# Performance work log

Hardware: AMD Instinct MI355X
Metric: run time of the kernel (lower is better)

Reference implementation:

```python
import jax, jax.numpy as jnp
import numpy as np

SEQ = 8          # sequence_size
C = 128          # in_channels / factor (hidden + input channels)
BN_EPS = 1e-5


def setup_inputs() -> dict:
    key = jax.random.key(0)
    k1, k2 = jax.random.split(key)
    x = jax.random.normal(k1, (32, C, 64, 64), dtype=jnp.float32)          # (B*T, C, H, W)
    w_conv = jax.random.normal(k2, (4 * C, 2 * C, 3, 3), dtype=jnp.float32) * 0.05  # OIHW
    b_conv = jnp.zeros((4 * C,), dtype=jnp.float32)
    gamma = jnp.ones((C,), dtype=jnp.float32)
    beta = jnp.zeros((C,), dtype=jnp.float32)
    run_mean = jnp.zeros((C,), dtype=jnp.float32)
    run_var = jnp.ones((C,), dtype=jnp.float32)
    return {"x": x, "w_conv": w_conv, "b_conv": b_conv, "gamma": gamma,
            "beta": beta, "run_mean": run_mean, "run_var": run_var}


def _convlstm_scan(x_seq, w_conv, b_conv):
    # x_seq: (B, T, C, H, W); zero initial (h, c) states (reset path)
    B, T, Cc, H, W = x_seq.shape
    h0 = jnp.zeros((B, Cc, H, W), x_seq.dtype)
    c0 = jnp.zeros((B, Cc, H, W), x_seq.dtype)

    def step(carry, x_t):
        h, c = carry
        z = jax.lax.conv_general_dilated(
            jnp.concatenate([x_t, h], axis=1), w_conv,
            window_strides=(1, 1), padding='SAME',
            dimension_numbers=('NCHW', 'OIHW', 'NCHW'))
        z = z + b_conv[None, :, None, None]
        i, f, o, g = jnp.split(z, 4, axis=1)
        c_next = jax.nn.sigmoid(f) * c + jax.nn.sigmoid(i) * jnp.tanh(g)
        h_next = jax.nn.sigmoid(o) * jnp.tanh(c_next)
        return (h_next, c_next), h_next

    _, hs = jax.lax.scan(step, (h0, c0), jnp.swapaxes(x_seq, 0, 1))  # hs: (T, B, C, H, W)
    return jnp.swapaxes(hs, 0, 1)  # (B, T, C, H, W)


def reference(x, w_conv, b_conv, gamma, beta, run_mean, run_var):
    BT, Cc, H, W = x.shape
    x_seq = x.reshape(BT // SEQ, SEQ, Cc, H, W)
    hs = _convlstm_scan(x_seq, w_conv, b_conv)           # (B, T, C, H, W)
    out = hs.reshape(-1, Cc, H, W)                        # (B*T, C, H, W)
    # BatchNorm2d (eval mode: running stats) + ReLU
    inv = jax.lax.rsqrt(run_var + BN_EPS)
    out = (out - run_mean[None, :, None, None]) * (inv * gamma)[None, :, None, None] \
          + beta[None, :, None, None]
    return jax.nn.relu(out)
```

## Files before the change

### kernel.cpp

```cpp
#include <hip/hip_runtime.h>
#include <hip/hip_bf16.h>
#include <math.h>

typedef __attribute__((ext_vector_type(8))) short bf16x8;
typedef __attribute__((ext_vector_type(4))) float f32x4;

#define FRAME_PAD (66*66*128)

#define GLOAD_LDS16(g, l) \
    __builtin_amdgcn_global_load_lds((const __attribute__((address_space(1))) void*)(g), \
                                     (__attribute__((address_space(3))) void*)(l), 16, 0, 0)

#define WAITV6    asm volatile("s_waitcnt vmcnt(6)" ::: "memory")
#define WAITV0    asm volatile("s_waitcnt vmcnt(0)" ::: "memory")
#define SBAR      __builtin_amdgcn_s_barrier()
#define MEMPIN    asm volatile("" ::: "memory")

__device__ __forceinline__ float sigmoidf_(float x) { return 1.0f / (1.0f + __expf(-x)); }
__device__ __forceinline__ float tanhf_(float x) {
    x = fminf(fmaxf(x, -15.0f), 15.0f);
    float e = __expf(2.0f * x);
    return (e - 1.0f) / (e + 1.0f);
}
__device__ __forceinline__ float b2f_(short u) {
    unsigned int v = ((unsigned int)(unsigned short)u) << 16;
    return __builtin_bit_cast(float, v);
}
__device__ __forceinline__ short f2b_(float f) {
    __hip_bfloat16 hb = __float2bfloat16(f);
    return *reinterpret_cast<short*>(&hb);
}

__global__ void wt_kernel(const float* __restrict__ w, __hip_bfloat16* __restrict__ wt)
{
    int idx = blockIdx.x * 256 + threadIdx.x;
    if (idx >= 9 * 512 * 256) return;
    int ic  = idx & 255;
    int n   = (idx >> 8) & 511;
    int tap = idx >> 17;
    int c = n >> 2, g = n & 3;
    int oc = g * 128 + c;
    wt[idx] = __float2bfloat16(w[((size_t)oc * 256 + (size_t)ic) * 9 + tap]);
}

__global__ void border_kernel(__hip_bfloat16* __restrict__ x_pad,
                              __hip_bfloat16* __restrict__ h_pad)
{
    const int fr = blockIdx.x;
    __hip_bfloat16* base = (fr < 32) ? x_pad + (size_t)fr * FRAME_PAD
                                     : h_pad + (size_t)(fr - 32) * FRAME_PAD;
    bf16x8 z = {};
    for (int u = threadIdx.x; u < 2112; u += 256) {
        int half = (u >= 1056) ? 1 : 0;
        int v = u - half * 1056;
        *(bf16x8*)(base + (size_t)(half * 65 * 66) * 128 + (size_t)v * 8) = z;
    }
    for (int u = threadIdx.x; u < 2048; u += 256) {
        int yy = 1 + (u >> 5);
        int r = u & 31;
        int side = r >> 4, c16 = r & 15;
        *(bf16x8*)(base + (size_t)(yy * 66 + side * 65) * 128 + (size_t)c16 * 8) = z;
    }
}

__global__ void xpose_kernel(const float* __restrict__ x, __hip_bfloat16* __restrict__ x_pad)
{
    __shared__ float tile[64][129];
    const int f = blockIdx.x >> 6;
    const int y = blockIdx.x & 63;
    const int tid = threadIdx.x;
    const float* src = x + (size_t)f * 524288 + (size_t)y * 64;
    #pragma unroll
    for (int it = 0; it < 8; ++it) {
        int c  = it * 16 + (tid >> 4);
        int xq = tid & 15;
        float4 v = *(const float4*)(src + (size_t)c * 4096 + xq * 4);
        tile[xq * 4 + 0][c] = v.x;
        tile[xq * 4 + 1][c] = v.y;
        tile[xq * 4 + 2][c] = v.z;
        tile[xq * 4 + 3][c] = v.w;
    }
    __syncthreads();
    __hip_bfloat16* dst = x_pad + (size_t)f * FRAME_PAD + (size_t)((y + 1) * 66 + 1) * 128;
    const int g = tid & 15;
    #pragma unroll
    for (int it = 0; it < 4; ++it) {
        int xr = it * 16 + (tid >> 4);
        bf16x8 o;
        #pragma unroll
        for (int e = 0; e < 8; ++e) o[e] = f2b_(tile[xr][g * 8 + e]);
        *(bf16x8*)(dst + (size_t)xr * 128 + g * 8) = o;
    }
}

template<bool T0>
__global__ __launch_bounds__(512, 2)
void conv_gemm(const __hip_bfloat16* __restrict__ x_pad,
               const __hip_bfloat16* __restrict__ h_pad,
               const __hip_bfloat16* __restrict__ wt,
               const float* __restrict__ bias,
               float* __restrict__ c_state, int t)
{
    __shared__ alignas(16) __hip_bfloat16 S_s[3][256 * 64];
    __shared__ alignas(16) __hip_bfloat16 W_s[3][128 * 64];
    const int tid  = threadIdx.x;
    const int wv   = tid >> 6;
    const int lane = tid & 63;
    const int KT   = T0 ? 18 : 36;

    const int F    = blockIdx.x;
    const int tile = (F >> 3) + (F & 7) * 32;
    const int n0   = (tile & 3) * 128;
    const int mblk = tile >> 2;
    const int b    = mblk >> 4;
    const int y0   = (mblk & 15) * 4;
    const int m0   = mblk * 256;

    const __hip_bfloat16* xf = x_pad + (size_t)(b * 8 + t) * FRAME_PAD;
    const __hip_bfloat16* hf = h_pad + (size_t)(b * 8 + (T0 ? 0 : t - 1)) * FRAME_PAD;

    int aOff[4], bOff[2];
    #pragma unroll
    for (int j = 0; j < 4; ++j) {
        int sid = j * 512 + tid;
        int row = sid >> 3;
        int q   = (sid & 7) ^ (row & 7);
        aOff[j] = ((y0 + (row >> 6)) * 66 + (row & 63)) * 128 + q * 8;
    }
    #pragma unroll
    for (int j = 0; j < 2; ++j) {
        int sid = j * 512 + tid;
        int row = sid >> 3;
        int q   = (sid & 7) ^ (row & 7);
        bOff[j] = (n0 + row) * 256 + q * 8;
    }

    auto STAGE = [&](__hip_bfloat16* Sl, __hip_bfloat16* Wl, int kt) {
        int tap, icq;
        const __hip_bfloat16* sb;
        if constexpr (T0) { tap = kt >> 1; icq = (kt & 1) * 64; sb = xf + icq; }
        else { tap = kt >> 2; icq = (kt & 3) * 64;
               sb = (icq < 128) ? (xf + icq) : (hf + (icq - 128)); }
        const int dy = tap / 3, dx = tap % 3;
        const __hip_bfloat16* a = sb + (dy * 66 + dx) * 128;
        #pragma unroll
        for (int j = 0; j < 4; ++j)
            GLOAD_LDS16(a + aOff[j], Sl + (size_t)(j * 512 + tid) * 8);
        const __hip_bfloat16* bsrc = wt + tap * 131072 + icq;
        #pragma unroll
        for (int j = 0; j < 2; ++j)
            GLOAD_LDS16(bsrc + bOff[j], Wl + (size_t)(j * 512 + tid) * 8);
    };

    const int wm = wv >> 1, wn = wv & 1;
    const int fr = lane & 15, fq = lane >> 4;
    const int slot = (fq ^ (fr & 7)) * 8;
    const int sOff0 = (wm * 64 + fr) * 64 + slot, sOff1 = sOff0 ^ 32;
    const int wOff0 = (wn * 64 + fr) * 64 + slot, wOff1 = wOff0 ^ 32;

    f32x4 acc[4][4] = {};

    __hip_bfloat16 *Sr = &S_s[0][0], *Sn = &S_s[1][0], *Sf = &S_s[2][0];
    __hip_bfloat16 *Wr = &W_s[0][0], *Wn = &W_s[1][0], *Wf = &W_s[2][0];

    STAGE(Sr, Wr, 0);
    STAGE(Sn, Wn, 1);

    #pragma unroll 1
    for (int kt = 0; kt < KT; ++kt) {
        if (kt < KT - 1) { WAITV6; } else { WAITV0; }
        SBAR;
        MEMPIN;
        if (kt < KT - 2) STAGE(Sf, Wf, kt + 2);

        bf16x8 w0[4], w1[4], s0[4], s1[4];
        #pragma unroll
        for (int ri = 0; ri < 4; ++ri) {
            w0[ri] = *(const bf16x8*)(Wr + wOff0 + ri * 1024);
            w1[ri] = *(const bf16x8*)(Wr + wOff1 + ri * 1024);
        }
        #pragma unroll
        for (int ci = 0; ci < 4; ++ci) {
            s0[ci] = *(const bf16x8*)(Sr + sOff0 + ci * 1024);
            s1[ci] = *(const bf16x8*)(Sr + sOff1 + ci * 1024);
        }
        __builtin_amdgcn_s_setprio(1);
        #pragma unroll
        for (int ri = 0; ri < 4; ++ri)
            #pragma unroll
            for (int ci = 0; ci < 4; ++ci)
                acc[ri][ci] = __builtin_amdgcn_mfma_f32_16x16x32_bf16(w0[ri], s0[ci], acc[ri][ci], 0, 0, 0);
        #pragma unroll
        for (int ri = 0; ri < 4; ++ri)
            #pragma unroll
            for (int ci = 0; ci < 4; ++ci)
                acc[ri][ci] = __builtin_amdgcn_mfma_f32_16x16x32_bf16(w1[ri], s1[ci], acc[ri][ci], 0, 0, 0);
        __builtin_amdgcn_s_setprio(0);

        __hip_bfloat16* tp = Sr; Sr = Sn; Sn = Sf; Sf = tp;
        __hip_bfloat16* tw = Wr; Wr = Wn; Wn = Wf; Wf = tw;
    }

    const int c0    = (n0 >> 2) + wn * 16;
    const int mcol0 = m0 + wm * 64 + fr;
    __hip_bfloat16* hout = (__hip_bfloat16*)h_pad + (size_t)(b * 8 + t) * FRAME_PAD;
    #pragma unroll
    for (int ri = 0; ri < 4; ++ri) {
        const int c = c0 + ri * 4 + fq;
        const float bi  = bias[c];
        const float bfv = bias[128 + c];
        const float bo  = bias[256 + c];
        const float bg  = bias[384 + c];
        float* csrow = c_state + (size_t)c * 16384;
        #pragma unroll
        for (int ci = 0; ci < 4; ++ci) {
            const int m = mcol0 + ci * 16;
            const int s = m & 4095;
            const float cold = T0 ? 0.0f : csrow[m];
            const float zi = acc[ri][ci][0] + bi;
            const float zf = acc[ri][ci][1] + bfv;
            const float zo = acc[ri][ci][2] + bo;
            const float zg = acc[ri][ci][3] + bg;
            const float cn = sigmoidf_(zf) * cold + sigmoidf_(zi) * tanhf_(zg);
            const float h  = sigmoidf_(zo) * tanhf_(cn);
            csrow[m] = cn;
            hout[(size_t)(((s >> 6) + 1) * 66 + (s & 63) + 1) * 128 + c] = __float2bfloat16(h);
        }
    }
}

__global__ void bn_out_kernel(const __hip_bfloat16* __restrict__ h_pad,
                              const float* __restrict__ gamma, const float* __restrict__ beta,
                              const float* __restrict__ rmean, const float* __restrict__ rvar,
                              float* __restrict__ out)
{
    __shared__ float tile[64][129];
    __shared__ float sc_s[128], sh_s[128];
    const int fo  = blockIdx.x >> 6;
    const int y   = blockIdx.x & 63;
    const int tid = threadIdx.x;
    if (tid < 128) {
        float sc = gamma[tid] * rsqrtf(rvar[tid] + 1e-5f);
        sc_s[tid] = sc;
        sh_s[tid] = beta[tid] - rmean[tid] * sc;
    }
    __syncthreads();
    const __hip_bfloat16* src =
        h_pad + (size_t)fo * FRAME_PAD + (size_t)((y + 1) * 66 + 1) * 128;
    const int g = tid & 15;
    float sc[8], sh[8];
    #pragma unroll
    for (int e = 0; e < 8; ++e) { sc[e] = sc_s[g * 8 + e]; sh[e] = sh_s[g * 8 + e]; }
    #pragma unroll
    for (int it = 0; it < 4; ++it) {
        int xr = it * 16 + (tid >> 4);
        bf16x8 v = *(const bf16x8*)(src + (size_t)xr * 128 + g * 8);
        #pragma unroll
        for (int e = 0; e < 8; ++e)
            tile[xr][g * 8 + e] = fmaxf(b2f_(v[e]) * sc[e] + sh[e], 0.0f);
    }
    __syncthreads();
    float* dst = out + (size_t)fo * 524288 + (size_t)y * 64;
    #pragma unroll
    for (int it = 0; it < 8; ++it) {
        int c  = it * 16 + (tid >> 4);
        int xq = tid & 15;
        float4 o;
        o.x = tile[xq * 4 + 0][c];
        o.y = tile[xq * 4 + 1][c];
        o.z = tile[xq * 4 + 2][c];
        o.w = tile[xq * 4 + 3][c];
        *(float4*)(dst + (size_t)c * 4096 + xq * 4) = o;
    }
}

extern "C" void kernel_launch(void* const* d_in, const int* in_sizes, int n_in,
                              void* d_out, int out_size, void* d_ws, size_t ws_size,
                              hipStream_t stream)
{
    const float* x      = (const float*)d_in[0];
    const float* w_conv = (const float*)d_in[1];
    const float* b_conv = (const float*)d_in[2];
    const float* gamma  = (const float*)d_in[3];
    const float* beta   = (const float*)d_in[4];
    const float* rmean  = (const float*)d_in[5];
    const float* rvar   = (const float*)d_in[6];
    float* out = (float*)d_out;

    if (ws_size < 82116608u) return;

    char* ws = (char*)d_ws;
    __hip_bfloat16* Wt    = (__hip_bfloat16*)(ws);
    __hip_bfloat16* x_pad = (__hip_bfloat16*)(ws + 2359296);
    __hip_bfloat16* h_pad = (__hip_bfloat16*)(ws + 38043648);
    float* c_state        = (float*)(ws + 73728000);

    wt_kernel<<<4608, 256, 0, stream>>>(w_conv, Wt);
    xpose_kernel<<<2048, 256, 0, stream>>>(x, x_pad);
    border_kernel<<<64, 256, 0, stream>>>(x_pad, h_pad);

    conv_gemm<true><<<256, 512, 0, stream>>>(x_pad, h_pad, Wt, b_conv, c_state, 0);
    for (int t = 1; t < 8; ++t)
        conv_gemm<false><<<256, 512, 0, stream>>>(x_pad, h_pad, Wt, b_conv, c_state, t);

    bn_out_kernel<<<2048, 256, 0, stream>>>(h_pad, gamma, beta, rmean, rvar, out);
}
```

Before: 424.6 us.

## Retile ConvLSTM conv GEMM to 128x128 blocks with 4 waves and K=32 steps

Shrinks each conv_gemm block from a 256x128 output tile with 8 waves and 64-wide K steps to a 128x128 tile with 4 waves and 32-wide K steps. The grid doubles to 512 blocks and LDS per block drops to about a third. The LDS swizzle, the load offsets and the vmcnt wait count are adjusted to match. The intent is two resident blocks per CU, which spreads the recurrent-step work more evenly and lets more blocks overlap. In exchange each block reuses weights less and hits a barrier twice as often per unit of MFMA work.

```diff
diff --git a/kernel.cpp b/kernel.cpp
--- a/kernel.cpp
+++ b/kernel.cpp
@@ -11,7 +11,7 @@
     __builtin_amdgcn_global_load_lds((const __attribute__((address_space(1))) void*)(g), \
                                      (__attribute__((address_space(3))) void*)(l), 16, 0, 0)
 
-#define WAITV6    asm volatile("s_waitcnt vmcnt(6)" ::: "memory")
+#define WAITV4    asm volatile("s_waitcnt vmcnt(4)" ::: "memory")
 #define WAITV0    asm volatile("s_waitcnt vmcnt(0)" ::: "memory")
 #define SBAR      __builtin_amdgcn_s_barrier()
 #define MEMPIN    asm volatile("" ::: "memory")
@@ -94,69 +94,63 @@
 }
 
 template<bool T0>
-__global__ __launch_bounds__(512, 2)
+__global__ __launch_bounds__(256, 2)
 void conv_gemm(const __hip_bfloat16* __restrict__ x_pad,
                const __hip_bfloat16* __restrict__ h_pad,
                const __hip_bfloat16* __restrict__ wt,
                const float* __restrict__ bias,
                float* __restrict__ c_state, int t)
 {
-    __shared__ alignas(16) __hip_bfloat16 S_s[3][256 * 64];
-    __shared__ alignas(16) __hip_bfloat16 W_s[3][128 * 64];
+    __shared__ alignas(16) __hip_bfloat16 S_s[3][128 * 32];
+    __shared__ alignas(16) __hip_bfloat16 W_s[3][128 * 32];
     const int tid  = threadIdx.x;
     const int wv   = tid >> 6;
     const int lane = tid & 63;
-    const int KT   = T0 ? 18 : 36;
+    const int KT   = T0 ? 36 : 72;
 
     const int F    = blockIdx.x;
-    const int tile = (F >> 3) + (F & 7) * 32;
+    const int tile = (F >> 3) + (F & 7) * 64;
     const int n0   = (tile & 3) * 128;
     const int mblk = tile >> 2;
-    const int b    = mblk >> 4;
-    const int y0   = (mblk & 15) * 4;
-    const int m0   = mblk * 256;
+    const int b    = mblk >> 5;
+    const int y0   = (mblk & 31) * 2;
+    const int m0   = mblk * 128;
 
     const __hip_bfloat16* xf = x_pad + (size_t)(b * 8 + t) * FRAME_PAD;
     const __hip_bfloat16* hf = h_pad + (size_t)(b * 8 + (T0 ? 0 : t - 1)) * FRAME_PAD;
 
-    int aOff[4], bOff[2];
-    #pragma unroll
-    for (int j = 0; j < 4; ++j) {
-        int sid = j * 512 + tid;
-        int row = sid >> 3;
-        int q   = (sid & 7) ^ (row & 7);
+    int aOff[2], bOff[2];
+    #pragma unroll
+    for (int j = 0; j < 2; ++j) {
+        int sid = j * 256 + tid;
+        int row = sid >> 2;
+        int q   = (sid & 3) ^ ((row >> 1) & 3);
         aOff[j] = ((y0 + (row >> 6)) * 66 + (row & 63)) * 128 + q * 8;
-    }
-    #pragma unroll
-    for (int j = 0; j < 2; ++j) {
-        int sid = j * 512 + tid;
-        int row = sid >> 3;
-        int q   = (sid & 7) ^ (row & 7);
         bOff[j] = (n0 + row) * 256 + q * 8;
     }
 
     auto STAGE = [&](__hip_bfloat16* Sl, __hip_bfloat16* Wl, int kt) {
         int tap, icq;
         const __hip_bfloat16* sb;
-        if constexpr (T0) { tap = kt >> 1; icq = (kt & 1) * 64; sb = xf + icq; }
-        else { tap = kt >> 2; icq = (kt & 3) * 64;
+        if constexpr (T0) { tap = kt >> 2; icq = (kt & 3) * 32; sb = xf + icq; }
+        else { tap = kt >> 3; icq = (kt & 7) * 32;
                sb = (icq < 128) ? (xf + icq) : (hf + (icq - 128)); }
         const int dy = tap / 3, dx = tap % 3;
         const __hip_bfloat16* a = sb + (dy * 66 + dx) * 128;
         #pragma unroll
-        for (int j = 0; j < 4; ++j)
-            GLOAD_LDS16(a + aOff[j], Sl + (size_t)(j * 512 + tid) * 8);
+        for (int j = 0; j < 2; ++j)
+            GLOAD_LDS16(a + aOff[j], Sl + (size_t)(j * 256 + tid) * 8);
         const __hip_bfloat16* bsrc = wt + tap * 131072 + icq;
         #pragma unroll
         for (int j = 0; j < 2; ++j)
-            GLOAD_LDS16(bsrc + bOff[j], Wl + (size_t)(j * 512 + tid) * 8);
+            GLOAD_LDS16(bsrc + bOff[j], Wl + (size_t)(j * 256 + tid) * 8);
     };
 
     const int wm = wv >> 1, wn = wv & 1;
     const int fr = lane & 15, fq = lane >> 4;
-    const int slot = (fq ^ (fr & 7)) * 8;
-    const int sOff0 = (wm * 64 + fr) * 64 + slot, sOff1 = sOff0 ^ 32;
-    const int wOff0 = (wn * 64 + fr) * 64 + slot, wOff1 = wOff0 ^ 32;
+    const int slot = (fq ^ ((fr >> 1) & 3)) * 8;
+    const int sA0 = (wm * 64 + fr) * 32 + slot;
+    const int wB0 = (wn * 64 + fr) * 32 + slot;
 
     f32x4 acc[4][4] = {};
 
@@ -168,33 +162,22 @@
 
     #pragma unroll 1
     for (int kt = 0; kt < KT; ++kt) {
-        if (kt < KT - 1) { WAITV6; } else { WAITV0; }
+        if (kt < KT - 1) { WAITV4; } else { WAITV0; }
         SBAR;
         MEMPIN;
         if (kt < KT - 2) STAGE(Sf, Wf, kt + 2);
 
-        bf16x8 w0[4], w1[4], s0[4], s1[4];
-        #pragma unroll
-        for (int ri = 0; ri < 4; ++ri) {
-            w0[ri] = *(const bf16x8*)(Wr + wOff0 + ri * 1024);
-            w1[ri] = *(const bf16x8*)(Wr + wOff1 + ri * 1024);
-        }
-        #pragma unroll
-        for (int ci = 0; ci < 4; ++ci) {
-            s0[ci] = *(const bf16x8*)(Sr + sOff0 + ci * 1024);
-            s1[ci] = *(const bf16x8*)(Sr + sOff1 + ci * 1024);
-        }
+        bf16x8 w[4], s[4];
+        #pragma unroll
+        for (int ri = 0; ri < 4; ++ri) w[ri] = *(const bf16x8*)(Wr + wB0 + ri * 512);
+        #pragma unroll
+        for (int ci = 0; ci < 4; ++ci) s[ci] = *(const bf16x8*)(Sr + sA0 + ci * 512);
         __builtin_amdgcn_s_setprio(1);
         #pragma unroll
         for (int ri = 0; ri < 4; ++ri)
             #pragma unroll
             for (int ci = 0; ci < 4; ++ci)
-                acc[ri][ci] = __builtin_amdgcn_mfma_f32_16x16x32_bf16(w0[ri], s0[ci], acc[ri][ci], 0, 0, 0);
-        #pragma unroll
-        for (int ri = 0; ri < 4; ++ri)
-            #pragma unroll
-            for (int ci = 0; ci < 4; ++ci)
-                acc[ri][ci] = __builtin_amdgcn_mfma_f32_16x16x32_bf16(w1[ri], s1[ci], acc[ri][ci], 0, 0, 0);
+                acc[ri][ci] = __builtin_amdgcn_mfma_f32_16x16x32_bf16(w[ri], s[ci], acc[ri][ci], 0, 0, 0);
         __builtin_amdgcn_s_setprio(0);
 
         __hip_bfloat16* tp = Sr; Sr = Sn; Sn = Sf; Sf = tp;
@@ -299,9 +282,9 @@
     xpose_kernel<<<2048, 256, 0, stream>>>(x, x_pad);
     border_kernel<<<64, 256, 0, stream>>>(x_pad, h_pad);
 
-    conv_gemm<true><<<256, 512, 0, stream>>>(x_pad, h_pad, Wt, b_conv, c_state, 0);
+    conv_gemm<true><<<512, 256, 0, stream>>>(x_pad, h_pad, Wt, b_conv, c_state, 0);
     for (int t = 1; t < 8; ++t)
-        conv_gemm<false><<<256, 512, 0, stream>>>(x_pad, h_pad, Wt, b_conv, c_state, t);
+        conv_gemm<false><<<512, 256, 0, stream>>>(x_pad, h_pad, Wt, b_conv, c_state, t);
 
     bn_out_kernel<<<2048, 256, 0, stream>>>(h_pad, gamma, beta, rmean, rvar, out);
 }
```

Result: slower. 443.9 us (+4.5%).

## Fuse BN+ReLU output into conv epilogue and switch to double-buffered LDS

Applied to the files above, without the earlier changes.

Removes the separate bn_out kernel by computing the BatchNorm scale/shift and ReLU in the conv_gemm epilogue, writing fp32 output directly. The LDS pipeline goes from triple to double buffering, with an added lgkmcnt wait and barrier mid-iteration so the next stage can load into the buffer just consumed while the second half of the MFMAs runs. This cuts LDS use, which may help occupancy, and saves a full read of h_pad. The trade-offs are an extra barrier per k-step and uncoalesced per-element fp32 output stores in the epilogue.

```diff
diff --git a/kernel.cpp b/kernel.cpp
--- a/kernel.cpp
+++ b/kernel.cpp
@@ -13,8 +13,8 @@
 
 #define WAITV6    asm volatile("s_waitcnt vmcnt(6)" ::: "memory")
 #define WAITV0    asm volatile("s_waitcnt vmcnt(0)" ::: "memory")
+#define WAITLGKM0 asm volatile("s_waitcnt lgkmcnt(0)" ::: "memory")
 #define SBAR      __builtin_amdgcn_s_barrier()
-#define MEMPIN    asm volatile("" ::: "memory")
 
 __device__ __forceinline__ float sigmoidf_(float x) { return 1.0f / (1.0f + __expf(-x)); }
 __device__ __forceinline__ float tanhf_(float x) {
@@ -99,10 +99,12 @@
                const __hip_bfloat16* __restrict__ h_pad,
                const __hip_bfloat16* __restrict__ wt,
                const float* __restrict__ bias,
-               float* __restrict__ c_state, int t)
-{
-    __shared__ alignas(16) __hip_bfloat16 S_s[3][256 * 64];
-    __shared__ alignas(16) __hip_bfloat16 W_s[3][128 * 64];
+               const float* __restrict__ gamma, const float* __restrict__ beta,
+               const float* __restrict__ rmean, const float* __restrict__ rvar,
+               float* __restrict__ c_state, float* __restrict__ out, int t)
+{
+    __shared__ alignas(16) __hip_bfloat16 S_s[2][256 * 64];
+    __shared__ alignas(16) __hip_bfloat16 W_s[2][128 * 64];
     const int tid  = threadIdx.x;
     const int wv   = tid >> 6;
     const int lane = tid & 63;
@@ -117,7 +119,8 @@
     const int m0   = mblk * 256;
 
     const __hip_bfloat16* xf = x_pad + (size_t)(b * 8 + t) * FRAME_PAD;
-    const __hip_bfloat16* hf = h_pad + (size_t)(b * 8 + (T0 ? 0 : t - 1)) * FRAME_PAD;
+    const __hip_bfloat16* hf = T0 ? xf
+                                  : h_pad + (size_t)(b * 8 + t - 1) * FRAME_PAD;
 
     int aOff[4], bOff[2];
     #pragma unroll
@@ -160,29 +163,19 @@
 
     f32x4 acc[4][4] = {};
 
-    __hip_bfloat16 *Sr = &S_s[0][0], *Sn = &S_s[1][0], *Sf = &S_s[2][0];
-    __hip_bfloat16 *Wr = &W_s[0][0], *Wn = &W_s[1][0], *Wf = &W_s[2][0];
-
-    STAGE(Sr, Wr, 0);
-    STAGE(Sn, Wn, 1);
-
-    #pragma unroll 1
-    for (int kt = 0; kt < KT; ++kt) {
+    auto ITER = [&](__hip_bfloat16* Sb, __hip_bfloat16* Wb, int kt) {
         if (kt < KT - 1) { WAITV6; } else { WAITV0; }
         SBAR;
-        MEMPIN;
-        if (kt < KT - 2) STAGE(Sf, Wf, kt + 2);
-
         bf16x8 w0[4], w1[4], s0[4], s1[4];
         #pragma unroll
         for (int ri = 0; ri < 4; ++ri) {
-            w0[ri] = *(const bf16x8*)(Wr + wOff0 + ri * 1024);
-            w1[ri] = *(const bf16x8*)(Wr + wOff1 + ri * 1024);
+            w0[ri] = *(const bf16x8*)(Wb + wOff0 + ri * 1024);
+            w1[ri] = *(const bf16x8*)(Wb + wOff1 + ri * 1024);
         }
         #pragma unroll
         for (int ci = 0; ci < 4; ++ci) {
-            s0[ci] = *(const bf16x8*)(Sr + sOff0 + ci * 1024);
-            s1[ci] = *(const bf16x8*)(Sr + sOff1 + ci * 1024);
+            s0[ci] = *(const bf16x8*)(Sb + sOff0 + ci * 1024);
+            s1[ci] = *(const bf16x8*)(Sb + sOff1 + ci * 1024);
         }
         __builtin_amdgcn_s_setprio(1);
         #pragma unroll
@@ -190,20 +183,32 @@
             #pragma unroll
             for (int ci = 0; ci < 4; ++ci)
                 acc[ri][ci] = __builtin_amdgcn_mfma_f32_16x16x32_bf16(w0[ri], s0[ci], acc[ri][ci], 0, 0, 0);
+        __builtin_amdgcn_s_setprio(0);
+        WAITLGKM0;
+        __builtin_amdgcn_sched_barrier(0);
+        SBAR;
+        if (kt < KT - 2) STAGE(Sb, Wb, kt + 2);
+        __builtin_amdgcn_s_setprio(1);
         #pragma unroll
         for (int ri = 0; ri < 4; ++ri)
             #pragma unroll
             for (int ci = 0; ci < 4; ++ci)
                 acc[ri][ci] = __builtin_amdgcn_mfma_f32_16x16x32_bf16(w1[ri], s1[ci], acc[ri][ci], 0, 0, 0);
         __builtin_amdgcn_s_setprio(0);
-
-        __hip_bfloat16* tp = Sr; Sr = Sn; Sn = Sf; Sf = tp;
-        __hip_bfloat16* tw = Wr; Wr = Wn; Wn = Wf; Wf = tw;
+    };
+
+    STAGE(S_s[0], W_s[0], 0);
+    STAGE(S_s[1], W_s[1], 1);
+    #pragma unroll 1
+    for (int kt = 0; kt < KT; kt += 2) {
+        ITER(S_s[0], W_s[0], kt);
+        ITER(S_s[1], W_s[1], kt + 1);
     }
 
     const int c0    = (n0 >> 2) + wn * 16;
     const int mcol0 = m0 + wm * 64 + fr;
     __hip_bfloat16* hout = (__hip_bfloat16*)h_pad + (size_t)(b * 8 + t) * FRAME_PAD;
+    float* oframe = out + (size_t)(b * 8 + t) * 524288;
     #pragma unroll
     for (int ri = 0; ri < 4; ++ri) {
         const int c = c0 + ri * 4 + fq;
@@ -211,6 +216,8 @@
         const float bfv = bias[128 + c];
         const float bo  = bias[256 + c];
         const float bg  = bias[384 + c];
+        const float scv = gamma[c] * rsqrtf(rvar[c] + 1e-5f);
+        const float shv = beta[c] - rmean[c] * scv;
         float* csrow = c_state + (size_t)c * 16384;
         #pragma unroll
         for (int ci = 0; ci < 4; ++ci) {
@@ -225,52 +232,8 @@
             const float h  = sigmoidf_(zo) * tanhf_(cn);
             csrow[m] = cn;
             hout[(size_t)(((s >> 6) + 1) * 66 + (s & 63) + 1) * 128 + c] = __float2bfloat16(h);
+            oframe[(size_t)c * 4096 + s] = fmaxf(h * scv + shv, 0.0f);
         }
-    }
-}
-
-__global__ void bn_out_kernel(const __hip_bfloat16* __restrict__ h_pad,
-                              const float* __restrict__ gamma, const float* __restrict__ beta,
-                              const float* __restrict__ rmean, const float* __restrict__ rvar,
-                              float* __restrict__ out)
-{
-    __shared__ float tile[64][129];
-    __shared__ float sc_s[128], sh_s[128];
-    const int fo  = blockIdx.x >> 6;
-    const int y   = blockIdx.x & 63;
-    const int tid = threadIdx.x;
-    if (tid < 128) {
-        float sc = gamma[tid] * rsqrtf(rvar[tid] + 1e-5f);
-        sc_s[tid] = sc;
-        sh_s[tid] = beta[tid] - rmean[tid] * sc;
-    }
-    __syncthreads();
-    const __hip_bfloat16* src =
-        h_pad + (size_t)fo * FRAME_PAD + (size_t)((y + 1) * 66 + 1) * 128;
-    const int g = tid & 15;
-    float sc[8], sh[8];
-    #pragma unroll
-    for (int e = 0; e < 8; ++e) { sc[e] = sc_s[g * 8 + e]; sh[e] = sh_s[g * 8 + e]; }
-    #pragma unroll
-    for (int it = 0; it < 4; ++it) {
-        int xr = it * 16 + (tid >> 4);
-        bf16x8 v = *(const bf16x8*)(src + (size_t)xr * 128 + g * 8);
-        #pragma unroll
-        for (int e = 0; e < 8; ++e)
-            tile[xr][g * 8 + e] = fmaxf(b2f_(v[e]) * sc[e] + sh[e], 0.0f);
-    }
-    __syncthreads();
-    float* dst = out + (size_t)fo * 524288 + (size_t)y * 64;
-    #pragma unroll
-    for (int it = 0; it < 8; ++it) {
-        int c  = it * 16 + (tid >> 4);
-        int xq = tid & 15;
-        float4 o;
-        o.x = tile[xq * 4 + 0][c];
-        o.y = tile[xq * 4 + 1][c];
-        o.z = tile[xq * 4 + 2][c];
-        o.w = tile[xq * 4 + 3][c];
-        *(float4*)(dst + (size_t)c * 4096 + xq * 4) = o;
     }
 }
 
@@ -299,9 +262,9 @@
     xpose_kernel<<<2048, 256, 0, stream>>>(x, x_pad);
     border_kernel<<<64, 256, 0, stream>>>(x_pad, h_pad);
 
-    conv_gemm<true><<<256, 512, 0, stream>>>(x_pad, h_pad, Wt, b_conv, c_state, 0);
+    conv_gemm<true><<<256, 512, 0, stream>>>(x_pad, h_pad, Wt, b_conv,
+                                             gamma, beta, rmean, rvar, c_state, out, 0);
     for (int t = 1; t < 8; ++t)
-        conv_gemm<false><<<256, 512, 0, stream>>>(x_pad, h_pad, Wt, b_conv, c_state, t);
-
-    bn_out_kernel<<<2048, 256, 0, stream>>>(h_pad, gamma, beta, rmean, rvar, out);
-}
+        conv_gemm<false><<<256, 512, 0, stream>>>(x_pad, h_pad, Wt, b_conv,
+                                                  gamma, beta, rmean, rvar, c_state, out, t);
+}
```

Result: faster. 354.1 us (-16.6%).
